# Kernel optimization log

Measured on AMD Instinct MI355X. Metric: run time of the kernel, lower is better.

Reference implementation:

```python
import jax, jax.numpy as jnp
import numpy as np

MAPSIZE = 256          # nearest power of two >= 224
BITS = 8               # log2(MAPSIZE)
PAD = (MAPSIZE - 224) // 2  # 16
WIBBLEDECAY = 2.0
EPSILON = 0.128
GREY = jnp.array([0.485, 0.45, 0.406], dtype=jnp.float32)


def fog_creator(fog_vars, bsize, mapsize, wibbledecay):
    """Diamond-square fractal noise with learnable perturbations (faithful port)."""
    m = jnp.zeros((bsize, mapsize, mapsize), dtype=jnp.float32)
    step = mapsize
    wibble = 1.0
    v = 0
    while step >= 2:
        h = step // 2
        # --- fillsquares: square centers = mean of 4 corners + wibble ---
        corner = m[:, 0:mapsize:step, 0:mapsize:step]          # (B, g, g)
        acc = corner + jnp.roll(corner, -1, axis=1)
        acc = acc + jnp.roll(acc, -1, axis=2)
        m = m.at[:, h:mapsize:step, h:mapsize:step].set(acc / 4.0 + wibble * fog_vars[v])
        v += 1
        # --- filldiamonds: diamond centers = mean of 4 neighbors + wibble ---
        dr = m[:, h:mapsize:step, h:mapsize:step]
        ul = m[:, 0:mapsize:step, 0:mapsize:step]
        lt = (dr + jnp.roll(dr, 1, axis=1)) + (ul + jnp.roll(ul, -1, axis=2))
        tt = (dr + jnp.roll(dr, 1, axis=2)) + (ul + jnp.roll(ul, -1, axis=1))
        m = m.at[:, 0:mapsize:step, h:mapsize:step].set(lt / 4.0 + wibble * fog_vars[v])
        v += 1
        m = m.at[:, h:mapsize:step, 0:mapsize:step].set(tt / 4.0 + wibble * fog_vars[v])
        v += 1
        step //= 2
        wibble /= wibbledecay
    return jnp.clip(jnp.abs(m), 0.0, 1.0)[:, None, :, :]  # (B, 1, M, M)


def apply_fog(inputs, fog):
    return inputs * (1.0 - fog) + fog * GREY.reshape(1, 3, 1, 1)


def setup_inputs() -> dict:
    key = jax.random.key(0)
    B = 256
    keys = jax.random.split(key, 3 * BITS + 1)
    inp = {"inputs": jax.random.uniform(keys[0], (B, 3, 224, 224), dtype=jnp.float32)}
    k = 1
    for i in range(BITS):
        g = 2 ** i
        for j in range(3):
            name = f"fog_{3 * i + j:02d}"
            inp[name] = EPSILON * jax.random.uniform(keys[k], (B, g, g), dtype=jnp.float32)
            k += 1
    return inp


def reference(inputs, fog_00, fog_01, fog_02, fog_03, fog_04, fog_05, fog_06, fog_07,
              fog_08, fog_09, fog_10, fog_11, fog_12, fog_13, fog_14, fog_15, fog_16,
              fog_17, fog_18, fog_19, fog_20, fog_21, fog_22, fog_23):
    fog_vars = [fog_00, fog_01, fog_02, fog_03, fog_04, fog_05, fog_06, fog_07,
                fog_08, fog_09, fog_10, fog_11, fog_12, fog_13, fog_14, fog_15,
                fog_16, fog_17, fog_18, fog_19, fog_20, fog_21, fog_22, fog_23]
    fog = fog_creator(fog_vars, inputs.shape[0], MAPSIZE, WIBBLEDECAY)
    fog = fog[:, :, PAD:-PAD, PAD:-PAD]  # crop 256 -> 224
    return apply_fog(inputs, fog)
```

## Files before the change

kernel.cpp:

```cpp
#include <hip/hip_runtime.h>


#define MAPB 128

struct FogPtrs { const float* f[24]; };

__global__ __launch_bounds__(256) void fog_coarse(FogPtrs fp, float* __restrict__ Cout) {
    __shared__ float Bm[MAPB * MAPB];
    const int b = blockIdx.x;
    const int t = threadIdx.x;
    if (t == 0) Bm[0] = 0.0f;
    __syncthreads();
    float w = 1.0f;
    for (int k = 0; k < 7; ++k) {
        const int n = 1 << k, mask = n - 1;
        const int S = MAPB >> k, H = S >> 1;
        const int nn = n * n;
        const float* __restrict__ f0 = fp.f[3 * k]     + b * nn;
        const float* __restrict__ f1 = fp.f[3 * k + 1] + b * nn;
        const float* __restrict__ f2 = fp.f[3 * k + 2] + b * nn;
        for (int idx = t; idx < nn; idx += 256) {
            const int i = idx >> k, j = idx & mask;
            const int i1 = (i + 1) & mask, j1 = (j + 1) & mask;
            const float c00 = Bm[i  * S * MAPB + j  * S];
            const float c10 = Bm[i1 * S * MAPB + j  * S];
            const float c01 = Bm[i  * S * MAPB + j1 * S];
            const float c11 = Bm[i1 * S * MAPB + j1 * S];
            Bm[(i * S + H) * MAPB + j * S + H] = (c00 + c10 + c01 + c11) * 0.25f + w * f0[idx];
        }
        __syncthreads();
        for (int idx = t; idx < nn; idx += 256) {
            const int i = idx >> k, j = idx & mask;
            const int i1 = (i + 1) & mask, j1 = (j + 1) & mask;
            const int im = (i - 1) & mask, jm = (j - 1) & mask;
            const float dij = Bm[(i  * S + H) * MAPB + j  * S + H];
            const float dmi = Bm[(im * S + H) * MAPB + j  * S + H];
            const float dmj = Bm[(i  * S + H) * MAPB + jm * S + H];
            const float c00 = Bm[i  * S * MAPB + j  * S];
            const float c01 = Bm[i  * S * MAPB + j1 * S];
            const float c10 = Bm[i1 * S * MAPB + j  * S];
            Bm[i * S * MAPB + j * S + H]       = (dij + dmi + c00 + c01) * 0.25f + w * f1[idx];
            Bm[(i * S + H) * MAPB + j * S]     = (dij + dmj + c00 + c10) * 0.25f + w * f2[idx];
        }
        __syncthreads();
        w *= 0.5f;
    }
    float4* __restrict__ dst = (float4*)(Cout + (size_t)b * (MAPB * MAPB));
    const float4* src = (const float4*)Bm;
    for (int idx = t; idx < MAPB * MAPB / 4; idx += 256) dst[idx] = src[idx];
}

__global__ __launch_bounds__(256) void fog_apply(
    const float* __restrict__ inp,
    const float* __restrict__ Cg,
    const float* __restrict__ f21, const float* __restrict__ f22, const float* __restrict__ f23,
    float* __restrict__ out)
{
    __shared__ float sC[18 * 128];
    __shared__ float sD[17 * 128];
    __shared__ float sF[32 * 224];
    const int b  = blockIdx.y;
    const int r0 = blockIdx.x * 32;
    const int t  = threadIdx.x;
    const int ci0 = (r0 >> 1) + 7;

    const float* __restrict__ Cb = Cg + (size_t)b * 16384 + ci0 * 128;
    for (int idx = t; idx < 18 * 128; idx += 256) sC[idx] = Cb[idx];
    __syncthreads();

    const float w7 = 0.0078125f;
    const float* __restrict__ f21b = f21 + (size_t)b * 16384 + ci0 * 128;
    for (int idx = t; idx < 17 * 128; idx += 256) {
        const int di = idx >> 7, j = idx & 127;
        const int j1 = (j + 1) & 127;
        sD[idx] = (sC[di * 128 + j] + sC[(di + 1) * 128 + j] +
                   sC[di * 128 + j1] + sC[(di + 1) * 128 + j1]) * 0.25f
                  + w7 * f21b[idx];
    }
    __syncthreads();

    const float* __restrict__ f22b = f22 + (size_t)b * 16384;
    const float* __restrict__ f23b = f23 + (size_t)b * 16384;
    for (int q = t; q < 16 * 112; q += 256) {
        const int qr = q / 112;
        const int qc = q - qr * 112;
        const int di = qr + 1;
        const int j  = qc + 8;
        const int gi = ci0 + di;
        const float c00 = sC[di * 128 + j];
        const float d11 = sD[di * 128 + j];
        const float mlt = (d11 + sD[(di - 1) * 128 + j] + c00 + sC[di * 128 + j + 1]) * 0.25f
                          + w7 * f22b[gi * 128 + j];
        const float mtt = (d11 + sD[di * 128 + j - 1] + c00 + sC[(di + 1) * 128 + j]) * 0.25f
                          + w7 * f23b[gi * 128 + j];
        const int fr = 2 * qr, fc = 2 * qc;
        float2 top, bot;
        top.x = fminf(fabsf(c00), 1.0f);
        top.y = fminf(fabsf(mlt), 1.0f);
        bot.x = fminf(fabsf(mtt), 1.0f);
        bot.y = fminf(fabsf(d11), 1.0f);
        *(float2*)&sF[fr * 224 + fc]       = top;
        *(float2*)&sF[(fr + 1) * 224 + fc] = bot;
    }
    __syncthreads();

    #pragma unroll
    for (int ch = 0; ch < 3; ++ch) {
        const float g = (ch == 0) ? 0.485f : ((ch == 1) ? 0.45f : 0.406f);
        const float4* __restrict__ ip = (const float4*)(inp + ((size_t)(b * 3 + ch) * 224 + r0) * 224);
        float4* __restrict__ op = (float4*)(out + ((size_t)(b * 3 + ch) * 224 + r0) * 224);
        for (int v = t; v < 32 * 56; v += 256) {
            float4 x = ip[v];
            const float4 f = *(const float4*)&sF[v * 4];
            float4 o;
            o.x = x.x * (1.0f - f.x) + f.x * g;
            o.y = x.y * (1.0f - f.y) + f.y * g;
            o.z = x.z * (1.0f - f.z) + f.z * g;
            o.w = x.w * (1.0f - f.w) + f.w * g;
            op[v] = o;
        }
    }
}

extern "C" void kernel_launch(void* const* d_in, const int* in_sizes, int n_in,
                              void* d_out, int out_size, void* d_ws, size_t ws_size,
                              hipStream_t stream) {
    (void)in_sizes; (void)n_in; (void)out_size; (void)ws_size;
    const float* inp = (const float*)d_in[0];
    FogPtrs fp;
    for (int v = 0; v < 24; ++v) fp.f[v] = (const float*)d_in[1 + v];
    float* Cg = (float*)d_ws;

    fog_coarse<<<dim3(256), dim3(256), 0, stream>>>(fp, Cg);
    fog_apply<<<dim3(7, 256), dim3(256), 0, stream>>>(
        inp, Cg, fp.f[21], fp.f[22], fp.f[23], (float*)d_out);
}
```

Measured before the change: 400.8 us.

## Apply fog directly from registers and widen coarse fog blocks to 1024 threads

```diff
diff --git a/kernel.cpp b/kernel.cpp
--- a/kernel.cpp
+++ b/kernel.cpp
@@ -5,7 +5,7 @@
 
 struct FogPtrs { const float* f[24]; };
 
-__global__ __launch_bounds__(256) void fog_coarse(FogPtrs fp, float* __restrict__ Cout) {
+__global__ __launch_bounds__(1024) void fog_coarse(FogPtrs fp, float* __restrict__ Cout) {
     __shared__ float Bm[MAPB * MAPB];
     const int b = blockIdx.x;
     const int t = threadIdx.x;
@@ -19,7 +19,7 @@
         const float* __restrict__ f0 = fp.f[3 * k]     + b * nn;
         const float* __restrict__ f1 = fp.f[3 * k + 1] + b * nn;
         const float* __restrict__ f2 = fp.f[3 * k + 2] + b * nn;
-        for (int idx = t; idx < nn; idx += 256) {
+        for (int idx = t; idx < nn; idx += 1024) {
             const int i = idx >> k, j = idx & mask;
             const int i1 = (i + 1) & mask, j1 = (j + 1) & mask;
             const float c00 = Bm[i  * S * MAPB + j  * S];
@@ -29,7 +29,7 @@
             Bm[(i * S + H) * MAPB + j * S + H] = (c00 + c10 + c01 + c11) * 0.25f + w * f0[idx];
         }
         __syncthreads();
-        for (int idx = t; idx < nn; idx += 256) {
+        for (int idx = t; idx < nn; idx += 1024) {
             const int i = idx >> k, j = idx & mask;
             const int i1 = (i + 1) & mask, j1 = (j + 1) & mask;
             const int im = (i - 1) & mask, jm = (j - 1) & mask;
@@ -47,7 +47,7 @@
     }
     float4* __restrict__ dst = (float4*)(Cout + (size_t)b * (MAPB * MAPB));
     const float4* src = (const float4*)Bm;
-    for (int idx = t; idx < MAPB * MAPB / 4; idx += 256) dst[idx] = src[idx];
+    for (int idx = t; idx < MAPB * MAPB / 4; idx += 1024) dst[idx] = src[idx];
 }
 
 __global__ __launch_bounds__(256) void fog_apply(
@@ -58,7 +58,6 @@
 {
     __shared__ float sC[18 * 128];
     __shared__ float sD[17 * 128];
-    __shared__ float sF[32 * 224];
     const int b  = blockIdx.y;
     const int r0 = blockIdx.x * 32;
     const int t  = threadIdx.x;
@@ -93,31 +92,26 @@
                           + w7 * f22b[gi * 128 + j];
         const float mtt = (d11 + sD[di * 128 + j - 1] + c00 + sC[(di + 1) * 128 + j]) * 0.25f
                           + w7 * f23b[gi * 128 + j];
-        const int fr = 2 * qr, fc = 2 * qc;
-        float2 top, bot;
-        top.x = fminf(fabsf(c00), 1.0f);
-        top.y = fminf(fabsf(mlt), 1.0f);
-        bot.x = fminf(fabsf(mtt), 1.0f);
-        bot.y = fminf(fabsf(d11), 1.0f);
-        *(float2*)&sF[fr * 224 + fc]       = top;
-        *(float2*)&sF[(fr + 1) * 224 + fc] = bot;
-    }
-    __syncthreads();
+        const float f00 = fminf(fabsf(c00), 1.0f);
+        const float f01 = fminf(fabsf(mlt), 1.0f);
+        const float f10 = fminf(fabsf(mtt), 1.0f);
+        const float f11 = fminf(fabsf(d11), 1.0f);
 
-    #pragma unroll
-    for (int ch = 0; ch < 3; ++ch) {
-        const float g = (ch == 0) ? 0.485f : ((ch == 1) ? 0.45f : 0.406f);
-        const float4* __restrict__ ip = (const float4*)(inp + ((size_t)(b * 3 + ch) * 224 + r0) * 224);
-        float4* __restrict__ op = (float4*)(out + ((size_t)(b * 3 + ch) * 224 + r0) * 224);
-        for (int v = t; v < 32 * 56; v += 256) {
-            float4 x = ip[v];
-            const float4 f = *(const float4*)&sF[v * 4];
-            float4 o;
-            o.x = x.x * (1.0f - f.x) + f.x * g;
-            o.y = x.y * (1.0f - f.y) + f.y * g;
-            o.z = x.z * (1.0f - f.z) + f.z * g;
-            o.w = x.w * (1.0f - f.w) + f.w * g;
-            op[v] = o;
+        const int row0 = r0 + 2 * qr;
+        const int col  = 2 * qc;
+        #pragma unroll
+        for (int ch = 0; ch < 3; ++ch) {
+            const float g = (ch == 0) ? 0.485f : ((ch == 1) ? 0.45f : 0.406f);
+            const size_t base = ((size_t)(b * 3 + ch) * 224 + row0) * 224 + col;
+            const float2 x0 = *(const float2*)(inp + base);
+            const float2 x1 = *(const float2*)(inp + base + 224);
+            float2 o0, o1;
+            o0.x = x0.x * (1.0f - f00) + f00 * g;
+            o0.y = x0.y * (1.0f - f01) + f01 * g;
+            o1.x = x1.x * (1.0f - f10) + f10 * g;
+            o1.y = x1.y * (1.0f - f11) + f11 * g;
+            *(float2*)(out + base)       = o0;
+            *(float2*)(out + base + 224) = o1;
         }
     }
 }
@@ -131,7 +125,7 @@
     for (int v = 0; v < 24; ++v) fp.f[v] = (const float*)d_in[1 + v];
     float* Cg = (float*)d_ws;
 
-    fog_coarse<<<dim3(256), dim3(256), 0, stream>>>(fp, Cg);
+    fog_coarse<<<dim3(256), dim3(1024), 0, stream>>>(fp, Cg);
     fog_apply<<<dim3(7, 256), dim3(256), 0, stream>>>(
         inp, Cg, fp.f[21], fp.f[22], fp.f[23], (float*)d_out);
 }
```

Measured after the change: 359.6 us. -10.3%, faster.
